# Kernel optimization log

Hardware: AMD Instinct MI355X
Metric: run time of the kernel (lower is better)

## Reference

```python
import jax, jax.numpy as jnp
import numpy as np
from jax import lax

B, T, D = 64, 512, 1024  # batch, seq_len, embDim == hiddenDim


def setup_inputs() -> dict:
    key = jax.random.key(0)
    ks = jax.random.split(key, 6)
    s = 1.0 / np.sqrt(D)
    return {
        "x": jax.random.normal(ks[0], (B, T, D), dtype=jnp.float32),
        "W_w": jax.random.uniform(ks[1], (D, D), jnp.float32, -s, s),
        "W_b": jax.random.uniform(ks[2], (D,), jnp.float32, -s, s),
        "U_w": jax.random.uniform(ks[3], (D, D), jnp.float32, -s, s),
        "U_b": jax.random.uniform(ks[4], (D,), jnp.float32, -s, s),
        "bias": jax.random.normal(ks[5], (1, D), dtype=jnp.float32),
    }


def reference(x, W_w, W_b, U_w, U_b, bias):
    # Precompute the input projection for all timesteps in one big GEMM:
    # wx[b,t,h] = x @ W_w^T + W_b  (torch Linear convention)
    wx = jnp.einsum('btd,hd->bth', x, W_w) + W_b  # (B, T, H)
    const = U_b + bias[0]  # fused per-step additive constant (H,)

    def step(h, wxt):
        # h: (B, H); wxt: (B, H)
        h_new = jnp.tanh(wxt + h @ U_w.T + const)
        return h_new, h_new

    h0 = jnp.zeros((x.shape[0], x.shape[2]), dtype=x.dtype)
    hT, outs = lax.scan(step, h0, jnp.swapaxes(wx, 0, 1))  # outs: (T, B, H)
    resultEmbs = jnp.swapaxes(outs, 0, 1)  # (B, T, H), batch_first=True
    return resultEmbs, hT[:, None, :]  # hx shape (B, 1, H) as in original
```

## Files before the change

### kernel.cpp

```cpp
#include <hip/hip_runtime.h>

#define BATCH 64
#define SEQT  512
#define DIM   1024

#define JB   32
#define BB   8
#define NJG  (DIM / JB)
#define NBG  (BATCH / BB)
#define NBLK (NJG * NBG)
#define NTHR 512
#define UPITCH 34

#define LDS_U    (DIM * UPITCH)
#define LDS_RED  (8 * 256)
#define LDS_VAL  (256)
#define LDS_H    (8 * 256)
#define LDS_BYTES ((LDS_U + LDS_RED + LDS_VAL + LDS_H) * 4)

typedef unsigned long long ull;
typedef float f4 __attribute__((ext_vector_type(4)));

union F2U {
    ull u;
    float f[2];
};

__global__ __launch_bounds__(256) void gemm_wx(const float* __restrict__ x,
                                               const float* __restrict__ Ww,
                                               const float* __restrict__ Wb,
                                               float* __restrict__ out) {
    __shared__ float As[16][64];
    __shared__ float Bs[16][64];

    const int tid = threadIdx.x;
    const int nb = blockIdx.x & 15;
    const int mb = blockIdx.x >> 4;
    const int m0 = mb * 64, n0 = nb * 64;
    const int tx = tid & 15, ty = tid >> 4;
    const int r0 = ty * 4, c0 = tx * 4;

    float acc[4][4] = {};

    const int lrow = tid >> 2;
    const int lk = (tid & 3) * 4;
    const float* xa = x + (size_t)(m0 + lrow) * DIM + lk;
    const float* wa = Ww + (size_t)(n0 + lrow) * DIM + lk;

    for (int kt = 0; kt < DIM / 16; ++kt) {
        float4 av = *(const float4*)xa;
        float4 bv = *(const float4*)wa;
        __syncthreads();
        As[lk + 0][lrow] = av.x; As[lk + 1][lrow] = av.y;
        As[lk + 2][lrow] = av.z; As[lk + 3][lrow] = av.w;
        Bs[lk + 0][lrow] = bv.x; Bs[lk + 1][lrow] = bv.y;
        Bs[lk + 2][lrow] = bv.z; Bs[lk + 3][lrow] = bv.w;
        __syncthreads();
#pragma unroll
        for (int kk = 0; kk < 16; ++kk) {
            float4 a = *(const float4*)&As[kk][r0];
            float4 b = *(const float4*)&Bs[kk][c0];
            acc[0][0] += a.x * b.x; acc[0][1] += a.x * b.y; acc[0][2] += a.x * b.z; acc[0][3] += a.x * b.w;
            acc[1][0] += a.y * b.x; acc[1][1] += a.y * b.y; acc[1][2] += a.y * b.z; acc[1][3] += a.y * b.w;
            acc[2][0] += a.z * b.x; acc[2][1] += a.z * b.y; acc[2][2] += a.z * b.z; acc[2][3] += a.z * b.w;
            acc[3][0] += a.w * b.x; acc[3][1] += a.w * b.y; acc[3][2] += a.w * b.z; acc[3][3] += a.w * b.w;
        }
        xa += 16; wa += 16;
    }

    float4 wb = *(const float4*)(Wb + n0 + c0);
#pragma unroll
    for (int i = 0; i < 4; ++i) {
        float4 o;
        o.x = acc[i][0] + wb.x; o.y = acc[i][1] + wb.y;
        o.z = acc[i][2] + wb.z; o.w = acc[i][3] + wb.w;
        *(float4*)(out + (size_t)(m0 + r0 + i) * DIM + n0 + c0) = o;
    }
}

__global__ __launch_bounds__(NTHR, 1) void rnn_scan3(
    const float* __restrict__ Uw,
    const float* __restrict__ Ub,
    const float* __restrict__ bias,
    float* __restrict__ out,
    float* __restrict__ h0,
    float* __restrict__ h1,
    unsigned* __restrict__ bar) {
    extern __shared__ float lds[];
    float* Ulds = lds;
    float* red  = lds + LDS_U;
    float* val  = red + LDS_RED;
    float* hbuf = val + LDS_VAL;

    const int tid = threadIdx.x;
    const int bg = blockIdx.x & 7;
    const int jg = blockIdx.x >> 3;
    const int j0 = jg * JB;
    const int b0 = bg * BB;

    {
        int c = tid & 31;
        int kc = (tid >> 5) << 6;
        const float* src = Uw + (size_t)(j0 + c) * DIM + kc;
#pragma unroll
        for (int i = 0; i < 16; ++i) {
            float4 v = *(const float4*)(src + i * 4);
            int k = kc + i * 4;
            Ulds[(k + 0) * UPITCH + c] = v.x;
            Ulds[(k + 1) * UPITCH + c] = v.y;
            Ulds[(k + 2) * UPITCH + c] = v.z;
            Ulds[(k + 3) * UPITCH + c] = v.w;
        }
    }

    float cst = 0.f;
    if (tid < 256) {
        int jl = tid & 31;
        cst = Ub[j0 + jl] + bias[j0 + jl];
    }
    __syncthreads();

    const int ksl = tid & 3;
    const int jt  = (tid >> 2) & 7;
    const int bt  = (tid >> 5) & 1;
    const int w   = tid >> 6;
    const int ln  = tid & 63;

    const float* uw_p0 = Ulds + (size_t)(128 * w + ksl) * UPITCH + jt * 4;
    const size_t colf = (size_t)bg * 8192;
    const size_t lf0 = (size_t)w * 1024 + (size_t)ln * 4;
    float* hstg = hbuf + w * 256 + ln * 4;
    const float* hrd = hbuf + w * 256 + ksl * 8 + bt * 4;
    unsigned* flagbase = bar + (size_t)bg * 1024;
    unsigned* myfp = flagbase + (size_t)(8 * w + (ln & 7)) * 16;

    ull junk = 0;

    for (int t = 0; t < SEQT; ++t) {
        const float* hc_col = ((t & 1) ? h1 : h0) + colf;
        float* hn_col = ((t & 1) ? h0 : h1) + colf;

        float wxv = 0.f;
        size_t oidx = 0;
        if (tid < 256) {
            int jl = tid & 31, bl = tid >> 5;
            oidx = ((size_t)(b0 + bl) * SEQT + t) * DIM + (j0 + jl);
            wxv = out[oidx];
        }

        if (t > 0) {
            unsigned want = (unsigned)t;
            unsigned f;
            do {
                f = want;
                if (ln < 8)
                    f = __hip_atomic_load(myfp, __ATOMIC_RELAXED, __HIP_MEMORY_SCOPE_AGENT);
            } while (__ballot(f < want));
        }
        asm volatile("" ::: "memory");
        __builtin_amdgcn_sched_barrier(0);

        const float* hp = hc_col + lf0;
        f4 hv0, hv1, hv2, hv3;
        asm volatile("global_load_dwordx4 %0, %1, off sc0 sc1" : "=v"(hv0) : "v"(hp));
        asm volatile("global_load_dwordx4 %0, %1, off sc0 sc1" : "=v"(hv1) : "v"(hp + 256));
        asm volatile("global_load_dwordx4 %0, %1, off sc0 sc1" : "=v"(hv2) : "v"(hp + 512));
        asm volatile("global_load_dwordx4 %0, %1, off sc0 sc1" : "=v"(hv3) : "v"(hp + 768));
        asm volatile("s_waitcnt vmcnt(0)"
                     : "+v"(hv0), "+v"(hv1), "+v"(hv2), "+v"(hv3)
                     :: "memory");
        __builtin_amdgcn_sched_barrier(0);

        float acc[4][4] = {};
        const float* up = uw_p0;

#pragma unroll
        for (int li = 0; li < 4; ++li) {
            f4 hv = (li == 0) ? hv0 : (li == 1) ? hv1 : (li == 2) ? hv2 : hv3;
            asm volatile("" ::: "memory");
            *(f4*)hstg = hv;
            asm volatile("" ::: "memory");
#pragma unroll
            for (int j = 0; j < 8; ++j) {
                float2 ua = *(const float2*)up;
                float2 ub = *(const float2*)(up + 2);
                f4 h4 = *(const f4*)(hrd + j * 32);
                acc[0][0] += ua.x * h4.x; acc[0][1] += ua.x * h4.y; acc[0][2] += ua.x * h4.z; acc[0][3] += ua.x * h4.w;
                acc[1][0] += ua.y * h4.x; acc[1][1] += ua.y * h4.y; acc[1][2] += ua.y * h4.z; acc[1][3] += ua.y * h4.w;
                acc[2][0] += ub.x * h4.x; acc[2][1] += ub.x * h4.y; acc[2][2] += ub.x * h4.z; acc[2][3] += ub.x * h4.w;
                acc[3][0] += ub.y * h4.x; acc[3][1] += ub.y * h4.y; acc[3][2] += ub.y * h4.z; acc[3][3] += ub.y * h4.w;
                up += 4 * UPITCH;
            }
        }

#pragma unroll
        for (int jj = 0; jj < 4; ++jj)
#pragma unroll
            for (int bb = 0; bb < 4; ++bb) {
                float v = acc[jj][bb];
                v += __shfl_xor(v, 1, 64);
                v += __shfl_xor(v, 2, 64);
                acc[jj][bb] = v;
            }
        if (ksl == 0) {
#pragma unroll
            for (int jj = 0; jj < 4; ++jj)
#pragma unroll
                for (int bb = 0; bb < 4; ++bb)
                    red[w * 256 + (bt * 4 + bb) * 32 + jt * 4 + jj] = acc[jj][bb];
        }
        __syncthreads();

        if (tid < 256) {
            float s = 0.f;
#pragma unroll
            for (int ww = 0; ww < 8; ++ww) s += red[ww * 256 + tid];
            float v = tanhf(wxv + s + cst);
            out[oidx] = v;
            val[tid] = v;
            if (t == SEQT - 1)
                out[(size_t)BATCH * SEQT * DIM + (size_t)(b0 + (tid >> 5)) * DIM + (j0 + (tid & 31))] = v;
        }
        __syncthreads();

        if (tid < 128) {
            int jl = tid >> 2, m = tid & 3;
            F2U p;
            p.f[0] = val[(2 * m + 0) * 32 + jl];
            p.f[1] = val[(2 * m + 1) * 32 + jl];
            ull old = __hip_atomic_exchange(
                (ull*)hn_col + (size_t)(j0 + jl) * 4 + m,
                p.u, __ATOMIC_RELAXED, __HIP_MEMORY_SCOPE_AGENT);
            junk ^= old;

            if (t < SEQT - 1) {
                __builtin_amdgcn_s_waitcnt(0);
                if ((tid & 63) == 0)
                    __hip_atomic_store(flagbase + ((size_t)jg * 2 + (tid >> 6)) * 16,
                                       (unsigned)(t + 1),
                                       __ATOMIC_RELAXED, __HIP_MEMORY_SCOPE_AGENT);
            }
        }
    }

    if (junk == 0xFFF00001FFF00002ULL) out[0] = -1.0f;
}

extern "C" void kernel_launch(void* const* d_in, const int* in_sizes, int n_in,
                              void* d_out, int out_size, void* d_ws, size_t ws_size,
                              hipStream_t stream) {
    const float* x    = (const float*)d_in[0];
    const float* W_w  = (const float*)d_in[1];
    const float* W_b  = (const float*)d_in[2];
    const float* U_w  = (const float*)d_in[3];
    const float* U_b  = (const float*)d_in[4];
    const float* bias = (const float*)d_in[5];
    float* out = (float*)d_out;

    unsigned* bar = (unsigned*)d_ws;
    float* h0 = (float*)((char*)d_ws + 65536);
    float* h1 = h0 + (size_t)DIM * BATCH;

    hipMemsetAsync(d_ws, 0, 65536 + 2 * (size_t)DIM * BATCH * sizeof(float), stream);

    gemm_wx<<<dim3((32768 / 64) * (DIM / 64)), dim3(256), 0, stream>>>(x, W_w, W_b, out);

    static bool attr_done = false;
    if (!attr_done) {
        hipFuncSetAttribute((const void*)rnn_scan3,
                            hipFuncAttributeMaxDynamicSharedMemorySize, LDS_BYTES);
        attr_done = true;
    }

    void* args[] = {(void*)&U_w, (void*)&U_b, (void*)&bias,
                    (void*)&out, (void*)&h0, (void*)&h1, (void*)&bar};
    hipLaunchCooperativeKernel((void*)rnn_scan3, dim3(NBLK), dim3(NTHR), args,
                               LDS_BYTES, stream);
}
```

Measured before the change: 3.891 ms.

## Hold U slice in registers, enlarge GEMM tiles, defer output store

Three separate changes. The recurrent scan now loads each thread's U weights from LDS into a 128-float register array once, then reuses the LDS region for reduction and h staging, which removes per-step LDS reads of U. The input-projection GEMM moves from 64x64 tiles with 4x4 per-thread outputs to 128x128 tiles with 8x8 per-thread outputs, raising arithmetic intensity. The per-step output store is moved after the h publish and flag write so it stays off the critical path. The cost is much higher register pressure in both kernels, with a risk of spills.

```diff
diff --git a/kernel.cpp b/kernel.cpp
--- a/kernel.cpp
+++ b/kernel.cpp
@@ -12,11 +12,7 @@
 #define NTHR 512
 #define UPITCH 34
 
-#define LDS_U    (DIM * UPITCH)
-#define LDS_RED  (8 * 256)
-#define LDS_VAL  (256)
-#define LDS_H    (8 * 256)
-#define LDS_BYTES ((LDS_U + LDS_RED + LDS_VAL + LDS_H) * 4)
+#define LDS_BYTES (DIM * UPITCH * 4)
 
 typedef unsigned long long ull;
 typedef float f4 __attribute__((ext_vector_type(4)));
@@ -30,51 +26,65 @@
                                                const float* __restrict__ Ww,
                                                const float* __restrict__ Wb,
                                                float* __restrict__ out) {
-    __shared__ float As[16][64];
-    __shared__ float Bs[16][64];
+    __shared__ float As[16][128];
+    __shared__ float Bs[16][128];
 
     const int tid = threadIdx.x;
-    const int nb = blockIdx.x & 15;
-    const int mb = blockIdx.x >> 4;
-    const int m0 = mb * 64, n0 = nb * 64;
+    const int nb = blockIdx.x & 7;
+    const int mb = blockIdx.x >> 3;
+    const int m0 = mb * 128, n0 = nb * 128;
     const int tx = tid & 15, ty = tid >> 4;
-    const int r0 = ty * 4, c0 = tx * 4;
-
-    float acc[4][4] = {};
-
-    const int lrow = tid >> 2;
-    const int lk = (tid & 3) * 4;
+
+    float acc[8][8] = {};
+
+    const int lrow = tid >> 1;
+    const int lk = (tid & 1) * 8;
     const float* xa = x + (size_t)(m0 + lrow) * DIM + lk;
     const float* wa = Ww + (size_t)(n0 + lrow) * DIM + lk;
 
     for (int kt = 0; kt < DIM / 16; ++kt) {
-        float4 av = *(const float4*)xa;
-        float4 bv = *(const float4*)wa;
+        float4 a0 = *(const float4*)xa, a1 = *(const float4*)(xa + 4);
+        float4 b0 = *(const float4*)wa, b1 = *(const float4*)(wa + 4);
         __syncthreads();
-        As[lk + 0][lrow] = av.x; As[lk + 1][lrow] = av.y;
-        As[lk + 2][lrow] = av.z; As[lk + 3][lrow] = av.w;
-        Bs[lk + 0][lrow] = bv.x; Bs[lk + 1][lrow] = bv.y;
-        Bs[lk + 2][lrow] = bv.z; Bs[lk + 3][lrow] = bv.w;
+        As[lk + 0][lrow] = a0.x; As[lk + 1][lrow] = a0.y;
+        As[lk + 2][lrow] = a0.z; As[lk + 3][lrow] = a0.w;
+        As[lk + 4][lrow] = a1.x; As[lk + 5][lrow] = a1.y;
+        As[lk + 6][lrow] = a1.z; As[lk + 7][lrow] = a1.w;
+        Bs[lk + 0][lrow] = b0.x; Bs[lk + 1][lrow] = b0.y;
+        Bs[lk + 2][lrow] = b0.z; Bs[lk + 3][lrow] = b0.w;
+        Bs[lk + 4][lrow] = b1.x; Bs[lk + 5][lrow] = b1.y;
+        Bs[lk + 6][lrow] = b1.z; Bs[lk + 7][lrow] = b1.w;
         __syncthreads();
 #pragma unroll
         for (int kk = 0; kk < 16; ++kk) {
-            float4 a = *(const float4*)&As[kk][r0];
-            float4 b = *(const float4*)&Bs[kk][c0];
-            acc[0][0] += a.x * b.x; acc[0][1] += a.x * b.y; acc[0][2] += a.x * b.z; acc[0][3] += a.x * b.w;
-            acc[1][0] += a.y * b.x; acc[1][1] += a.y * b.y; acc[1][2] += a.y * b.z; acc[1][3] += a.y * b.w;
-            acc[2][0] += a.z * b.x; acc[2][1] += a.z * b.y; acc[2][2] += a.z * b.z; acc[2][3] += a.z * b.w;
-            acc[3][0] += a.w * b.x; acc[3][1] += a.w * b.y; acc[3][2] += a.w * b.z; acc[3][3] += a.w * b.w;
+            float4 ax0 = *(const float4*)&As[kk][ty * 4];
+            float4 ax1 = *(const float4*)&As[kk][ty * 4 + 64];
+            float4 bx0 = *(const float4*)&Bs[kk][tx * 4];
+            float4 bx1 = *(const float4*)&Bs[kk][tx * 4 + 64];
+            float ar[8] = {ax0.x, ax0.y, ax0.z, ax0.w, ax1.x, ax1.y, ax1.z, ax1.w};
+            float br[8] = {bx0.x, bx0.y, bx0.z, bx0.w, bx1.x, bx1.y, bx1.z, bx1.w};
+#pragma unroll
+            for (int r = 0; r < 8; ++r)
+#pragma unroll
+                for (int c = 0; c < 8; ++c)
+                    acc[r][c] += ar[r] * br[c];
         }
         xa += 16; wa += 16;
     }
 
-    float4 wb = *(const float4*)(Wb + n0 + c0);
-#pragma unroll
-    for (int i = 0; i < 4; ++i) {
-        float4 o;
-        o.x = acc[i][0] + wb.x; o.y = acc[i][1] + wb.y;
-        o.z = acc[i][2] + wb.z; o.w = acc[i][3] + wb.w;
-        *(float4*)(out + (size_t)(m0 + r0 + i) * DIM + n0 + c0) = o;
+    float4 wb0 = *(const float4*)(Wb + n0 + tx * 4);
+    float4 wb1 = *(const float4*)(Wb + n0 + tx * 4 + 64);
+#pragma unroll
+    for (int r = 0; r < 8; ++r) {
+        int row = m0 + ty * 4 + (r & 3) + ((r >> 2) << 6);
+        float* op = out + (size_t)row * DIM + n0;
+        float4 o0, o1;
+        o0.x = acc[r][0] + wb0.x; o0.y = acc[r][1] + wb0.y;
+        o0.z = acc[r][2] + wb0.z; o0.w = acc[r][3] + wb0.w;
+        o1.x = acc[r][4] + wb1.x; o1.y = acc[r][5] + wb1.y;
+        o1.z = acc[r][6] + wb1.z; o1.w = acc[r][7] + wb1.w;
+        *(float4*)(op + tx * 4) = o0;
+        *(float4*)(op + tx * 4 + 64) = o1;
     }
 }
 
@@ -88,9 +98,9 @@
     unsigned* __restrict__ bar) {
     extern __shared__ float lds[];
     float* Ulds = lds;
-    float* red  = lds + LDS_U;
-    float* val  = red + LDS_RED;
-    float* hbuf = val + LDS_VAL;
+    float* red  = lds;
+    float* val  = lds + 2048;
+    float* hbuf = lds + 2304;
 
     const int tid = threadIdx.x;
     const int bg = blockIdx.x & 7;
@@ -126,7 +136,19 @@
     const int w   = tid >> 6;
     const int ln  = tid & 63;
 
-    const float* uw_p0 = Ulds + (size_t)(128 * w + ksl) * UPITCH + jt * 4;
+    float ur[32][4];
+    {
+        const float* up = Ulds + (size_t)(128 * w + ksl) * UPITCH + jt * 4;
+#pragma unroll
+        for (int i = 0; i < 32; ++i) {
+            float2 a = *(const float2*)up;
+            float2 b = *(const float2*)(up + 2);
+            ur[i][0] = a.x; ur[i][1] = a.y; ur[i][2] = b.x; ur[i][3] = b.y;
+            up += 4 * UPITCH;
+        }
+    }
+    __syncthreads();
+
     const size_t colf = (size_t)bg * 8192;
     const size_t lf0 = (size_t)w * 1024 + (size_t)ln * 4;
     float* hstg = hbuf + w * 256 + ln * 4;
@@ -172,7 +194,6 @@
         __builtin_amdgcn_sched_barrier(0);
 
         float acc[4][4] = {};
-        const float* up = uw_p0;
 
 #pragma unroll
         for (int li = 0; li < 4; ++li) {
@@ -182,14 +203,12 @@
             asm volatile("" ::: "memory");
 #pragma unroll
             for (int j = 0; j < 8; ++j) {
-                float2 ua = *(const float2*)up;
-                float2 ub = *(const float2*)(up + 2);
+                const int i = li * 8 + j;
                 f4 h4 = *(const f4*)(hrd + j * 32);
-                acc[0][0] += ua.x * h4.x; acc[0][1] += ua.x * h4.y; acc[0][2] += ua.x * h4.z; acc[0][3] += ua.x * h4.w;
-                acc[1][0] += ua.y * h4.x; acc[1][1] += ua.y * h4.y; acc[1][2] += ua.y * h4.z; acc[1][3] += ua.y * h4.w;
-                acc[2][0] += ub.x * h4.x; acc[2][1] += ub.x * h4.y; acc[2][2] += ub.x * h4.z; acc[2][3] += ub.x * h4.w;
-                acc[3][0] += ub.y * h4.x; acc[3][1] += ub.y * h4.y; acc[3][2] += ub.y * h4.z; acc[3][3] += ub.y * h4.w;
-                up += 4 * UPITCH;
+                acc[0][0] += ur[i][0] * h4.x; acc[0][1] += ur[i][0] * h4.y; acc[0][2] += ur[i][0] * h4.z; acc[0][3] += ur[i][0] * h4.w;
+                acc[1][0] += ur[i][1] * h4.x; acc[1][1] += ur[i][1] * h4.y; acc[1][2] += ur[i][1] * h4.z; acc[1][3] += ur[i][1] * h4.w;
+                acc[2][0] += ur[i][2] * h4.x; acc[2][1] += ur[i][2] * h4.y; acc[2][2] += ur[i][2] * h4.z; acc[2][3] += ur[i][2] * h4.w;
+                acc[3][0] += ur[i][3] * h4.x; acc[3][1] += ur[i][3] * h4.y; acc[3][2] += ur[i][3] * h4.z; acc[3][3] += ur[i][3] * h4.w;
             }
         }
 
@@ -211,12 +230,12 @@
         }
         __syncthreads();
 
+        float v = 0.f;
         if (tid < 256) {
             float s = 0.f;
 #pragma unroll
             for (int ww = 0; ww < 8; ++ww) s += red[ww * 256 + tid];
-            float v = tanhf(wxv + s + cst);
-            out[oidx] = v;
+            v = tanhf(wxv + s + cst);
             val[tid] = v;
             if (t == SEQT - 1)
                 out[(size_t)BATCH * SEQT * DIM + (size_t)(b0 + (tid >> 5)) * DIM + (j0 + (tid & 31))] = v;
@@ -241,6 +260,8 @@
                                        __ATOMIC_RELAXED, __HIP_MEMORY_SCOPE_AGENT);
             }
         }
+        asm volatile("" ::: "memory");
+        if (tid < 256) out[oidx] = v;
     }
 
     if (junk == 0xFFF00001FFF00002ULL) out[0] = -1.0f;
@@ -263,7 +284,7 @@
 
     hipMemsetAsync(d_ws, 0, 65536 + 2 * (size_t)DIM * BATCH * sizeof(float), stream);
 
-    gemm_wx<<<dim3((32768 / 64) * (DIM / 64)), dim3(256), 0, stream>>>(x, W_w, W_b, out);
+    gemm_wx<<<dim3((32768 / 128) * (DIM / 128)), dim3(256), 0, stream>>>(x, W_w, W_b, out);
 
     static bool attr_done = false;
     if (!attr_done) {
```

Measured after the change: 3.127 ms. 19.6% less time.
